# Kernel tuning notes

Measured on AMD Instinct MI355X. Metric: run time of the kernel, lower is better.

The kernel has to match this reference:

```python
import jax, jax.numpy as jnp
import numpy as np

N_NODES = 100000
N_EDGES = 1600000
D_IN = 128
D_HID = 128


def setup_inputs() -> dict:
    key = jax.random.key(0)
    ks = jax.random.split(key, 8)
    x = jax.random.normal(ks[0], (N_NODES, D_IN), dtype=jnp.float32)
    edge_index = jax.random.randint(ks[1], (2, N_EDGES), 0, N_NODES, dtype=jnp.int64)
    s = 1.0 / np.sqrt(D_IN)
    W_root1 = jax.random.normal(ks[2], (D_IN, D_HID), dtype=jnp.float32) * s
    W_rel1 = jax.random.normal(ks[3], (D_IN, D_HID), dtype=jnp.float32) * s
    b1 = jnp.zeros((D_HID,), dtype=jnp.float32)
    sh = 1.0 / np.sqrt(D_HID)
    W_root2 = jax.random.normal(ks[4], (D_HID, D_HID), dtype=jnp.float32) * sh
    W_rel2 = jax.random.normal(ks[5], (D_HID, D_HID), dtype=jnp.float32) * sh
    b2 = jnp.zeros((D_HID,), dtype=jnp.float32)
    return {"x": x, "edge_index": edge_index, "W_root1": W_root1, "W_rel1": W_rel1,
            "b1": b1, "W_root2": W_root2, "W_rel2": W_rel2, "b2": b2}


def graph_conv(x, src, dst, W_root, W_rel, b):
    # PyG GraphConv: out_i = x_i @ W_root + (sum_{j in N(i)} x_j) @ W_rel + b
    agg = jax.ops.segment_sum(x[src], dst, num_segments=N_NODES)  # [N, d]
    return x @ W_root + agg @ W_rel + b


def reference(x, edge_index, W_root1, W_rel1, b1, W_root2, W_rel2, b2):
    src, dst = edge_index[0], edge_index[1]
    h = jax.nn.relu(graph_conv(x, src, dst, W_root1, W_rel1, b1))
    # dropout is identity in eval mode (reference baseline)
    h = jax.nn.relu(graph_conv(h, src, dst, W_root2, W_rel2, b2))
    return h
```

## Files before the change

### kernel.cpp

```cpp
#include <hip/hip_runtime.h>

#define D 128
#define KTOT 256
#define GM 128
#define LPAD 8
#define LSTR (KTOT + LPAD)

#define EB1   8192
#define BKT_W 64
#define WIN   1024
#define EMAX  8192
#define HB1MAX 2048

typedef __attribute__((ext_vector_type(8))) short bf16x8;
typedef __attribute__((ext_vector_type(4))) float f32x4;
typedef __attribute__((ext_vector_type(4))) unsigned int u32x4;

__device__ __forceinline__ unsigned short f2b(float f) {
    unsigned int u = __float_as_uint(f);
    u += 0x7fffu + ((u >> 16) & 1u);
    return (unsigned short)(u >> 16);
}
__device__ __forceinline__ float blo(unsigned int u) { return __uint_as_float(u << 16); }
__device__ __forceinline__ float bhi(unsigned int u) { return __uint_as_float(u & 0xffff0000u); }

__global__ __launch_bounds__(256) void pack_count_kernel(
    const void* __restrict__ ei, unsigned int* __restrict__ pk,
    unsigned short* __restrict__ bkt, int n_edges, int nb1,
    int* __restrict__ C)
{
    __shared__ int h[HB1MAX];
    for (int i = threadIdx.x; i < nb1; i += 256) h[i] = 0;

    const unsigned int* eiu = (const unsigned int*)ei;
    const int l = threadIdx.x & 63;
    unsigned int w0 = eiu[2 * l + 1];
    unsigned int w1 = eiu[2 * (l + 64) + 1];
    const int is64 = __all((w0 | w1) == 0u);
    __syncthreads();

    const int e0 = blockIdx.x * EB1;
    const int e1 = min(e0 + EB1, n_edges);
    for (int e = e0 + threadIdx.x; e < e1; e += 256) {
        int s, d;
        if (is64) {
            const long long* p = (const long long*)ei;
            s = (int)p[e]; d = (int)p[n_edges + e];
        } else {
            const int* p = (const int*)ei;
            s = p[e]; d = p[n_edges + e];
        }
        pk[e]  = ((unsigned int)s << 6) | (unsigned int)(d & (BKT_W - 1));
        int b = d >> 6;
        bkt[e] = (unsigned short)b;
        atomicAdd(&h[b], 1);
    }
    __syncthreads();
    int* out = C + (long long)blockIdx.x * nb1;
    for (int i = threadIdx.x; i < nb1; i += 256) out[i] = h[i];
}

__global__ __launch_bounds__(1024) void scanA_kernel(
    const int* __restrict__ C, int* __restrict__ Cs,
    int* __restrict__ blockSums, int L, int nb1, int nblk1)
{
    __shared__ int sm[1024];
    const int tid = threadIdx.x;
    const int i = blockIdx.x * 1024 + tid;
    int v = 0;
    if (i < L) {
        int b = i / nblk1, k = i - b * nblk1;
        v = C[(long long)k * nb1 + b];
    }
    int val = v;
    sm[tid] = val;
    __syncthreads();
    for (int off = 1; off < 1024; off <<= 1) {
        int t = (tid >= off) ? sm[tid - off] : 0;
        __syncthreads();
        val += t;
        sm[tid] = val;
        __syncthreads();
    }
    if (i < L) Cs[i] = val - v;
    if (tid == 1023) blockSums[blockIdx.x] = val;
}

__global__ __launch_bounds__(1024) void scan2_kernel(int* __restrict__ bs, int nb)
{
    __shared__ int sm[1024];
    int t = threadIdx.x;
    int v = (t < nb) ? bs[t] : 0;
    int val = v;
    sm[t] = val;
    __syncthreads();
    for (int off = 1; off < 1024; off <<= 1) {
        int u = (t >= off) ? sm[t - off] : 0;
        __syncthreads();
        val += u;
        sm[t] = val;
        __syncthreads();
    }
    if (t < nb) bs[t] = val - v;
}

__global__ __launch_bounds__(1024) void scan3_kernel(
    int* __restrict__ arr, const int* __restrict__ blockSums, int n)
{
    const int i = blockIdx.x * 1024 + threadIdx.x;
    if (i >= n) return;
    arr[i] += blockSums[blockIdx.x];
}

__global__ __launch_bounds__(256) void s1_scatter_kernel(
    const unsigned short* __restrict__ bkt, const unsigned int* __restrict__ pk,
    const int* __restrict__ Cs, unsigned int* __restrict__ sorted,
    int n_edges, int nb1, int nblk1, int lo)
{
    __shared__ int cur[WIN];
    const int hi = min(lo + WIN, nb1);
    for (int t = threadIdx.x; t < hi - lo; t += 256)
        cur[t] = Cs[(long long)(lo + t) * nblk1 + blockIdx.x];
    __syncthreads();
    const int e0 = blockIdx.x * EB1;
    const int e1 = min(e0 + EB1, n_edges);
    for (int e = e0 + threadIdx.x; e < e1; e += 256) {
        int b = bkt[e];
        if (b >= lo && b < hi) {
            int pos = atomicAdd(&cur[b - lo], 1);
            sorted[pos] = pk[e];
        }
    }
}

__global__ __launch_bounds__(256) void bucket_sort_kernel(
    unsigned int* __restrict__ sorted, const int* __restrict__ Cs,
    int n_edges, int n_nodes, int nb1, int nblk1, int* __restrict__ row_end)
{
    __shared__ unsigned int lpk[EMAX];
    __shared__ int h64[BKT_W], excl[BKT_W + 1], cur[BKT_W];
    const int b = blockIdx.x;
    const int t = threadIdx.x;
    const int base = Cs[(long long)b * nblk1];
    const int nextb = (b + 1 < nb1) ? Cs[(long long)(b + 1) * nblk1] : n_edges;
    const int cnt = min(nextb - base, EMAX);

    if (t < BKT_W) h64[t] = 0;
    for (int i = t; i < cnt; i += 256) lpk[i] = sorted[base + i];
    __syncthreads();
    for (int i = t; i < cnt; i += 256) atomicAdd(&h64[lpk[i] & (BKT_W - 1)], 1);
    __syncthreads();
    if (t == 0) {
        int run = 0;
        #pragma unroll
        for (int i = 0; i < BKT_W; ++i) { excl[i] = run; run += h64[i]; }
        excl[BKT_W] = run;
    }
    __syncthreads();
    const int node0 = b * BKT_W;
    const int bins = min(BKT_W, n_nodes - node0);
    if (t < bins) row_end[node0 + t] = base + excl[t + 1];
    if (t < BKT_W) cur[t] = excl[t];
    __syncthreads();
    for (int i = t; i < cnt; i += 256) {
        unsigned int p = lpk[i];
        int pos = atomicAdd(&cur[p & (BKT_W - 1)], 1);
        sorted[base + pos] = p >> 6;
    }
}

__global__ __launch_bounds__(256) void prep_kernel(
    const float* __restrict__ x, unsigned short* __restrict__ Xb,
    long long nelem, int nbcvt,
    const float* __restrict__ Wr1, const float* __restrict__ Wl1,
    unsigned short* __restrict__ Wt1,
    const float* __restrict__ Wr2, const float* __restrict__ Wl2,
    unsigned short* __restrict__ Wt2)
{
    const int b = blockIdx.x;
    if (b < nbcvt) {
        long long i = ((long long)b * 256 + threadIdx.x) * 8;
        if (i >= nelem) return;
        float4 a = *(const float4*)(x + i);
        float4 c2 = *(const float4*)(x + i + 4);
        bf16x8 v;
        v[0] = (short)f2b(a.x);  v[1] = (short)f2b(a.y);
        v[2] = (short)f2b(a.z);  v[3] = (short)f2b(a.w);
        v[4] = (short)f2b(c2.x); v[5] = (short)f2b(c2.y);
        v[6] = (short)f2b(c2.z); v[7] = (short)f2b(c2.w);
        *(bf16x8*)(Xb + i) = v;
    } else {
        const int cb = b - nbcvt;
        const float* Wr = (cb < 128) ? Wr1 : Wr2;
        const float* Wl = (cb < 128) ? Wl1 : Wl2;
        unsigned short* Wt = (cb < 128) ? Wt1 : Wt2;
        const int c = cb & 127;
        const int k = threadIdx.x;
        float v = (k < 128) ? Wr[k * D + c] : Wl[(k - 128) * D + c];
        Wt[c * KTOT + k] = f2b(v);
    }
}

#define ACC8(u) { a0 += blo(u.x); a1 += bhi(u.x); a2 += blo(u.y); a3 += bhi(u.y); \
                  a4 += blo(u.z); a5 += bhi(u.z); a6 += blo(u.w); a7 += bhi(u.w); }

__global__ __launch_bounds__(256) void agg_kernel(
    const unsigned short* __restrict__ src, const int* __restrict__ sorted_src,
    const int* __restrict__ row_end, unsigned short* __restrict__ dst, int n)
{
    const int node = blockIdx.x * 4 + (threadIdx.x >> 6);
    if (node >= n) return;
    const int lane = threadIdx.x & 63;
    const int j = lane >> 4;
    const int c = (lane & 15) * 8;
    const int beg = node ? row_end[node - 1] : 0;
    const int end = row_end[node];

    float a0 = 0.f, a1 = 0.f, a2 = 0.f, a3 = 0.f,
          a4 = 0.f, a5 = 0.f, a6 = 0.f, a7 = 0.f;

    int i = beg + j;
    for (; i + 12 < end; i += 16) {
        int s0 = __builtin_nontemporal_load(&sorted_src[i]);
        int s1 = __builtin_nontemporal_load(&sorted_src[i + 4]);
        int s2 = __builtin_nontemporal_load(&sorted_src[i + 8]);
        int s3 = __builtin_nontemporal_load(&sorted_src[i + 12]);
        uint4 u0 = *(const uint4*)(src + (long long)s0 * D + c);
        uint4 u1 = *(const uint4*)(src + (long long)s1 * D + c);
        uint4 u2 = *(const uint4*)(src + (long long)s2 * D + c);
        uint4 u3 = *(const uint4*)(src + (long long)s3 * D + c);
        ACC8(u0); ACC8(u1); ACC8(u2); ACC8(u3);
    }
    for (; i < end; i += 4) {
        int s0 = __builtin_nontemporal_load(&sorted_src[i]);
        uint4 u0 = *(const uint4*)(src + (long long)s0 * D + c);
        ACC8(u0);
    }

    a0 += __shfl_xor(a0, 16); a1 += __shfl_xor(a1, 16);
    a2 += __shfl_xor(a2, 16); a3 += __shfl_xor(a3, 16);
    a4 += __shfl_xor(a4, 16); a5 += __shfl_xor(a5, 16);
    a6 += __shfl_xor(a6, 16); a7 += __shfl_xor(a7, 16);
    a0 += __shfl_xor(a0, 32); a1 += __shfl_xor(a1, 32);
    a2 += __shfl_xor(a2, 32); a3 += __shfl_xor(a3, 32);
    a4 += __shfl_xor(a4, 32); a5 += __shfl_xor(a5, 32);
    a6 += __shfl_xor(a6, 32); a7 += __shfl_xor(a7, 32);

    if (j == 0) {
        u32x4 p;
        p[0] = (unsigned int)f2b(a0) | ((unsigned int)f2b(a1) << 16);
        p[1] = (unsigned int)f2b(a2) | ((unsigned int)f2b(a3) << 16);
        p[2] = (unsigned int)f2b(a4) | ((unsigned int)f2b(a5) << 16);
        p[3] = (unsigned int)f2b(a6) | ((unsigned int)f2b(a7) << 16);
        u32x4* addr = (u32x4*)(dst + (long long)node * D + c);
        __builtin_nontemporal_store(p, addr);
    }
}

template <int OUT_BF16>
__global__ __launch_bounds__(512) void gemm_kernel(
    const unsigned short* __restrict__ Xop, const unsigned short* __restrict__ Aop,
    const unsigned short* __restrict__ Wt, const float* __restrict__ bias,
    void* outp, int n)
{
    __shared__ short sW[D][LSTR];
    const int tid = threadIdx.x;
    const int r0 = blockIdx.x * GM;

    for (int i = 0; i < 8; ++i) {
        int idx = tid + i * 512;
        int r = idx >> 5, c8 = idx & 31;
        bf16x8 w = *(const bf16x8*)(Wt + r * KTOT + c8 * 8);
        *(bf16x8*)&sW[r][c8 * 8] = w;
    }
    __syncthreads();

    const int w    = tid >> 6;
    const int lane = tid & 63;
    const int lr   = lane & 15;
    const int lk   = (lane >> 4) * 8;
    const int row  = r0 + w * 16 + lr;
    const bool rok = (row < n);

    f32x4 acc[8];
    #pragma unroll
    for (int ct = 0; ct < 8; ++ct) acc[ct] = (f32x4){0.f, 0.f, 0.f, 0.f};

    #pragma unroll
    for (int ks = 0; ks < 8; ++ks) {
        bf16x8 a = {};
        if (rok) {
            const unsigned short* base = (ks < 4) ? Xop : Aop;
            a = *(const bf16x8*)(base + (long long)row * D + (ks & 3) * 32 + lk);
        }
        #pragma unroll
        for (int ct = 0; ct < 8; ++ct) {
            bf16x8 bf = *(const bf16x8*)&sW[ct * 16 + lr][ks * 32 + lk];
            acc[ct] = __builtin_amdgcn_mfma_f32_16x16x32_bf16(a, bf, acc[ct], 0, 0, 0);
        }
    }

    const int rbase = r0 + w * 16 + (lane >> 4) * 4;
    #pragma unroll
    for (int ct = 0; ct < 8; ++ct) {
        const int col = ct * 16 + lr;
        const float bv = bias[col];
        #pragma unroll
        for (int j = 0; j < 4; ++j) {
            int orow = rbase + j;
            if (orow < n) {
                float val = fmaxf(acc[ct][j] + bv, 0.f);
                if (OUT_BF16) {
                    ((unsigned short*)outp)[(long long)orow * D + col] = f2b(val);
                } else {
                    ((float*)outp)[(long long)orow * D + col] = val;
                }
            }
        }
    }
}

static inline size_t align_up(size_t v, size_t a) { return (v + a - 1) & ~(a - 1); }

extern "C" void kernel_launch(void* const* d_in, const int* in_sizes, int n_in,
                              void* d_out, int out_size, void* d_ws, size_t ws_size,
                              hipStream_t stream) {
    const float* x   = (const float*)d_in[0];
    const void*  ei  = d_in[1];
    const float* Wr1 = (const float*)d_in[2];
    const float* Wl1 = (const float*)d_in[3];
    const float* b1  = (const float*)d_in[4];
    const float* Wr2 = (const float*)d_in[5];
    const float* Wl2 = (const float*)d_in[6];
    const float* b2  = (const float*)d_in[7];
    float* out = (float*)d_out;

    const int n_nodes = in_sizes[0] / D;
    const int n_edges = in_sizes[1] / 2;

    const int nb1   = (n_nodes + BKT_W - 1) / BKT_W;
    const int nblk1 = (n_edges + EB1 - 1) / EB1;
    const int L     = nb1 * nblk1;
    const int npass = (nb1 + WIN - 1) / WIN;
    const int nbL   = (L + 1023) / 1024;

    char* ws = (char*)d_ws;
    size_t off_rs   = 0;
    size_t off_bs   = align_up(off_rs + 4 * (size_t)(n_nodes + 1), 256);
    size_t off_ssrc = align_up(off_bs + 4 * 1024, 256);
    size_t off_wt1  = align_up(off_ssrc + 4 * (size_t)n_edges, 256);
    size_t off_wt2  = align_up(off_wt1 + 2 * (size_t)D * KTOT, 256);
    size_t off_xb   = align_up(off_wt2 + 2 * (size_t)D * KTOT, 256);
    size_t off_ab   = align_up(off_xb + 2 * (size_t)n_nodes * D, 256);

    int* row_end         = (int*)(ws + off_rs);
    int* blockSums       = (int*)(ws + off_bs);
    unsigned int* sorted = (unsigned int*)(ws + off_ssrc);
    unsigned short* Wt1  = (unsigned short*)(ws + off_wt1);
    unsigned short* Wt2  = (unsigned short*)(ws + off_wt2);
    unsigned short* Xb   = (unsigned short*)(ws + off_xb);
    unsigned short* Ab   = (unsigned short*)(ws + off_ab);
    unsigned int*   pk  = (unsigned int*)(ws + off_xb);
    unsigned short* bkt = (unsigned short*)(pk + n_edges);
    int* C  = (int*)(ws + off_ab);
    int* Cs = C + L;

    const int gemm_blocks = (n_nodes + GM - 1) / GM;
    const int agg_blocks  = (n_nodes + 3) / 4;
    const long long nfeat = (long long)n_nodes * D;
    const int nbcvt = (int)((nfeat / 8 + 255) / 256);

    pack_count_kernel<<<nblk1, 256, 0, stream>>>(ei, pk, bkt, n_edges, nb1, C);
    scanA_kernel<<<nbL, 1024, 0, stream>>>(C, Cs, blockSums, L, nb1, nblk1);
    scan2_kernel<<<1, 1024, 0, stream>>>(blockSums, nbL);
    scan3_kernel<<<nbL, 1024, 0, stream>>>(Cs, blockSums, L);
    for (int p = 0; p < npass; ++p) {
        s1_scatter_kernel<<<nblk1, 256, 0, stream>>>(
            bkt, pk, Cs, sorted, n_edges, nb1, nblk1, p * WIN);
    }

    prep_kernel<<<nbcvt + 256, 256, 0, stream>>>(
        x, Xb, nfeat, nbcvt, Wr1, Wl1, Wt1, Wr2, Wl2, Wt2);

    bucket_sort_kernel<<<nb1, 256, 0, stream>>>(
        sorted, Cs, n_edges, n_nodes, nb1, nblk1, row_end);

    agg_kernel<<<agg_blocks, 256, 0, stream>>>(
        Xb, (const int*)sorted, row_end, Ab, n_nodes);
    gemm_kernel<1><<<gemm_blocks, 512, 0, stream>>>(Xb, Ab, Wt1, b1, Ab, n_nodes);

    agg_kernel<<<agg_blocks, 256, 0, stream>>>(
        Ab, (const int*)sorted, row_end, Xb, n_nodes);
    gemm_kernel<0><<<gemm_blocks, 512, 0, stream>>>(Ab, Xb, Wt2, b2, out, n_nodes);
}
```

Baseline: 272.1 us.

## Merge preprocessing kernels to cut launches; drop nontemporal hints in aggregation

Folds the single-block block-sum scan into scan3: each block now reduces its preceding block sums itself. The multi-pass scatter loop becomes one launch over all windows, and bucket sort is merged with the bf16 conversion and weight-transpose kernel. Together these cut several kernel launches and the serial gaps between them. The aggregation kernel also switches from nontemporal loads and stores to ordinary ones so the index and output data can stay in cache, at the cost of redundant block-sum reductions and a larger fused kernel with more shared memory per block.

```diff
diff --git a/kernel.cpp b/kernel.cpp
--- a/kernel.cpp
+++ b/kernel.cpp
@@ -14,7 +14,6 @@
 
 typedef __attribute__((ext_vector_type(8))) short bf16x8;
 typedef __attribute__((ext_vector_type(4))) float f32x4;
-typedef __attribute__((ext_vector_type(4))) unsigned int u32x4;
 
 __device__ __forceinline__ unsigned short f2b(float f) {
     unsigned int u = __float_as_uint(f);
@@ -86,43 +85,36 @@
     if (tid == 1023) blockSums[blockIdx.x] = val;
 }
 
-__global__ __launch_bounds__(1024) void scan2_kernel(int* __restrict__ bs, int nb)
-{
-    __shared__ int sm[1024];
-    int t = threadIdx.x;
-    int v = (t < nb) ? bs[t] : 0;
-    int val = v;
-    sm[t] = val;
-    __syncthreads();
-    for (int off = 1; off < 1024; off <<= 1) {
-        int u = (t >= off) ? sm[t - off] : 0;
-        __syncthreads();
-        val += u;
-        sm[t] = val;
-        __syncthreads();
-    }
-    if (t < nb) bs[t] = val - v;
-}
-
 __global__ __launch_bounds__(1024) void scan3_kernel(
     int* __restrict__ arr, const int* __restrict__ blockSums, int n)
 {
-    const int i = blockIdx.x * 1024 + threadIdx.x;
-    if (i >= n) return;
-    arr[i] += blockSums[blockIdx.x];
+    __shared__ int sm[1024];
+    const int tid = threadIdx.x;
+    sm[tid] = (tid < blockIdx.x) ? blockSums[tid] : 0;
+    __syncthreads();
+    #pragma unroll
+    for (int off = 512; off > 0; off >>= 1) {
+        if (tid < off) sm[tid] += sm[tid + off];
+        __syncthreads();
+    }
+    const int i = blockIdx.x * 1024 + tid;
+    if (i < n) arr[i] += sm[0];
 }
 
 __global__ __launch_bounds__(256) void s1_scatter_kernel(
     const unsigned short* __restrict__ bkt, const unsigned int* __restrict__ pk,
     const int* __restrict__ Cs, unsigned int* __restrict__ sorted,
-    int n_edges, int nb1, int nblk1, int lo)
+    int n_edges, int nb1, int nblk1)
 {
     __shared__ int cur[WIN];
-    const int hi = min(lo + WIN, nb1);
+    const int win = blockIdx.x / nblk1;
+    const int blk = blockIdx.x - win * nblk1;
+    const int lo  = win * WIN;
+    const int hi  = min(lo + WIN, nb1);
     for (int t = threadIdx.x; t < hi - lo; t += 256)
-        cur[t] = Cs[(long long)(lo + t) * nblk1 + blockIdx.x];
-    __syncthreads();
-    const int e0 = blockIdx.x * EB1;
+        cur[t] = Cs[(long long)(lo + t) * nblk1 + blk];
+    __syncthreads();
+    const int e0 = blk * EB1;
     const int e1 = min(e0 + EB1, n_edges);
     for (int e = e0 + threadIdx.x; e < e1; e += 256) {
         int b = bkt[e];
@@ -133,43 +125,9 @@
     }
 }
 
-__global__ __launch_bounds__(256) void bucket_sort_kernel(
+__global__ __launch_bounds__(256) void sort_prep_kernel(
     unsigned int* __restrict__ sorted, const int* __restrict__ Cs,
-    int n_edges, int n_nodes, int nb1, int nblk1, int* __restrict__ row_end)
-{
-    __shared__ unsigned int lpk[EMAX];
-    __shared__ int h64[BKT_W], excl[BKT_W + 1], cur[BKT_W];
-    const int b = blockIdx.x;
-    const int t = threadIdx.x;
-    const int base = Cs[(long long)b * nblk1];
-    const int nextb = (b + 1 < nb1) ? Cs[(long long)(b + 1) * nblk1] : n_edges;
-    const int cnt = min(nextb - base, EMAX);
-
-    if (t < BKT_W) h64[t] = 0;
-    for (int i = t; i < cnt; i += 256) lpk[i] = sorted[base + i];
-    __syncthreads();
-    for (int i = t; i < cnt; i += 256) atomicAdd(&h64[lpk[i] & (BKT_W - 1)], 1);
-    __syncthreads();
-    if (t == 0) {
-        int run = 0;
-        #pragma unroll
-        for (int i = 0; i < BKT_W; ++i) { excl[i] = run; run += h64[i]; }
-        excl[BKT_W] = run;
-    }
-    __syncthreads();
-    const int node0 = b * BKT_W;
-    const int bins = min(BKT_W, n_nodes - node0);
-    if (t < bins) row_end[node0 + t] = base + excl[t + 1];
-    if (t < BKT_W) cur[t] = excl[t];
-    __syncthreads();
-    for (int i = t; i < cnt; i += 256) {
-        unsigned int p = lpk[i];
-        int pos = atomicAdd(&cur[p & (BKT_W - 1)], 1);
-        sorted[base + pos] = p >> 6;
-    }
-}
-
-__global__ __launch_bounds__(256) void prep_kernel(
+    int n_edges, int n_nodes, int nb1, int nblk1, int* __restrict__ row_end,
     const float* __restrict__ x, unsigned short* __restrict__ Xb,
     long long nelem, int nbcvt,
     const float* __restrict__ Wr1, const float* __restrict__ Wl1,
@@ -177,9 +135,41 @@
     const float* __restrict__ Wr2, const float* __restrict__ Wl2,
     unsigned short* __restrict__ Wt2)
 {
-    const int b = blockIdx.x;
-    if (b < nbcvt) {
-        long long i = ((long long)b * 256 + threadIdx.x) * 8;
+    __shared__ unsigned int lpk[EMAX];
+    __shared__ int h64[BKT_W], excl[BKT_W + 1], cur[BKT_W];
+    const int bid = blockIdx.x;
+    const int t = threadIdx.x;
+
+    if (bid < nb1) {
+        const int b = bid;
+        const int base = Cs[(long long)b * nblk1];
+        const int nextb = (b + 1 < nb1) ? Cs[(long long)(b + 1) * nblk1] : n_edges;
+        const int cnt = min(nextb - base, EMAX);
+
+        if (t < BKT_W) h64[t] = 0;
+        for (int i = t; i < cnt; i += 256) lpk[i] = sorted[base + i];
+        __syncthreads();
+        for (int i = t; i < cnt; i += 256) atomicAdd(&h64[lpk[i] & (BKT_W - 1)], 1);
+        __syncthreads();
+        if (t == 0) {
+            int run = 0;
+            #pragma unroll
+            for (int i = 0; i < BKT_W; ++i) { excl[i] = run; run += h64[i]; }
+            excl[BKT_W] = run;
+        }
+        __syncthreads();
+        const int node0 = b * BKT_W;
+        const int bins = min(BKT_W, n_nodes - node0);
+        if (t < bins) row_end[node0 + t] = base + excl[t + 1];
+        if (t < BKT_W) cur[t] = excl[t];
+        __syncthreads();
+        for (int i = t; i < cnt; i += 256) {
+            unsigned int p = lpk[i];
+            int pos = atomicAdd(&cur[p & (BKT_W - 1)], 1);
+            sorted[base + pos] = p >> 6;
+        }
+    } else if (bid < nb1 + nbcvt) {
+        const long long i = ((long long)(bid - nb1) * 256 + t) * 8;
         if (i >= nelem) return;
         float4 a = *(const float4*)(x + i);
         float4 c2 = *(const float4*)(x + i + 4);
@@ -190,12 +180,12 @@
         v[6] = (short)f2b(c2.z); v[7] = (short)f2b(c2.w);
         *(bf16x8*)(Xb + i) = v;
     } else {
-        const int cb = b - nbcvt;
+        const int cb = bid - nb1 - nbcvt;
         const float* Wr = (cb < 128) ? Wr1 : Wr2;
         const float* Wl = (cb < 128) ? Wl1 : Wl2;
         unsigned short* Wt = (cb < 128) ? Wt1 : Wt2;
         const int c = cb & 127;
-        const int k = threadIdx.x;
+        const int k = t;
         float v = (k < 128) ? Wr[k * D + c] : Wl[(k - 128) * D + c];
         Wt[c * KTOT + k] = f2b(v);
     }
@@ -221,10 +211,10 @@
 
     int i = beg + j;
     for (; i + 12 < end; i += 16) {
-        int s0 = __builtin_nontemporal_load(&sorted_src[i]);
-        int s1 = __builtin_nontemporal_load(&sorted_src[i + 4]);
-        int s2 = __builtin_nontemporal_load(&sorted_src[i + 8]);
-        int s3 = __builtin_nontemporal_load(&sorted_src[i + 12]);
+        int s0 = sorted_src[i];
+        int s1 = sorted_src[i + 4];
+        int s2 = sorted_src[i + 8];
+        int s3 = sorted_src[i + 12];
         uint4 u0 = *(const uint4*)(src + (long long)s0 * D + c);
         uint4 u1 = *(const uint4*)(src + (long long)s1 * D + c);
         uint4 u2 = *(const uint4*)(src + (long long)s2 * D + c);
@@ -232,7 +222,7 @@
         ACC8(u0); ACC8(u1); ACC8(u2); ACC8(u3);
     }
     for (; i < end; i += 4) {
-        int s0 = __builtin_nontemporal_load(&sorted_src[i]);
+        int s0 = sorted_src[i];
         uint4 u0 = *(const uint4*)(src + (long long)s0 * D + c);
         ACC8(u0);
     }
@@ -247,13 +237,12 @@
     a6 += __shfl_xor(a6, 32); a7 += __shfl_xor(a7, 32);
 
     if (j == 0) {
-        u32x4 p;
-        p[0] = (unsigned int)f2b(a0) | ((unsigned int)f2b(a1) << 16);
-        p[1] = (unsigned int)f2b(a2) | ((unsigned int)f2b(a3) << 16);
-        p[2] = (unsigned int)f2b(a4) | ((unsigned int)f2b(a5) << 16);
-        p[3] = (unsigned int)f2b(a6) | ((unsigned int)f2b(a7) << 16);
-        u32x4* addr = (u32x4*)(dst + (long long)node * D + c);
-        __builtin_nontemporal_store(p, addr);
+        uint4 p;
+        p.x = (unsigned int)f2b(a0) | ((unsigned int)f2b(a1) << 16);
+        p.y = (unsigned int)f2b(a2) | ((unsigned int)f2b(a3) << 16);
+        p.z = (unsigned int)f2b(a4) | ((unsigned int)f2b(a5) << 16);
+        p.w = (unsigned int)f2b(a6) | ((unsigned int)f2b(a7) << 16);
+        *(uint4*)(dst + (long long)node * D + c) = p;
     }
 }
 
@@ -372,18 +361,13 @@
 
     pack_count_kernel<<<nblk1, 256, 0, stream>>>(ei, pk, bkt, n_edges, nb1, C);
     scanA_kernel<<<nbL, 1024, 0, stream>>>(C, Cs, blockSums, L, nb1, nblk1);
-    scan2_kernel<<<1, 1024, 0, stream>>>(blockSums, nbL);
     scan3_kernel<<<nbL, 1024, 0, stream>>>(Cs, blockSums, L);
-    for (int p = 0; p < npass; ++p) {
-        s1_scatter_kernel<<<nblk1, 256, 0, stream>>>(
-            bkt, pk, Cs, sorted, n_edges, nb1, nblk1, p * WIN);
-    }
-
-    prep_kernel<<<nbcvt + 256, 256, 0, stream>>>(
+    s1_scatter_kernel<<<nblk1 * npass, 256, 0, stream>>>(
+        bkt, pk, Cs, sorted, n_edges, nb1, nblk1);
+
+    sort_prep_kernel<<<nb1 + nbcvt + 256, 256, 0, stream>>>(
+        sorted, Cs, n_edges, n_nodes, nb1, nblk1, row_end,
         x, Xb, nfeat, nbcvt, Wr1, Wl1, Wt1, Wr2, Wl2, Wt2);
-
-    bucket_sort_kernel<<<nb1, 256, 0, stream>>>(
-        sorted, Cs, n_edges, n_nodes, nb1, nblk1, row_end);
 
     agg_kernel<<<agg_blocks, 256, 0, stream>>>(
         Xb, (const int*)sorted, row_end, Ab, n_nodes);
```

Measured after the change: 237.7 us, median of 2. -12.6%, faster.
